# Performance work log

Measured on AMD Instinct MI355X. Metric: run time of the kernel, lower is better.

## Reference

```python
import jax, jax.numpy as jnp
import numpy as np
from jax import lax

D_MODEL = 256
SCALES = 3
DM2 = 2 * D_MODEL            # 512, inner d_model of each Mamba2
EXPAND = 2
D_INNER = EXPAND * DM2       # 1024
HEADDIM = 64                 # Mamba2 default
NHEADS = D_INNER // HEADDIM  # 16
DSTATE = 128
DCONV = 4
D_IN_PROJ = 2 * D_INNER + 2 * DSTATE + NHEADS  # 2320
CONV_CH = D_INNER + 2 * DSTATE                 # 1280


def layernorm(x, g, b, eps=1e-5):
    mu = x.mean(-1, keepdims=True)
    v = ((x - mu) ** 2).mean(-1, keepdims=True)
    return (x - mu) * lax.rsqrt(v + eps) * g + b


def mamba2(x, Win, convw, convb, dtb, Alog, Dh, normw, Wout):
    # x: [B, L, DM2]
    Bb, L, _ = x.shape
    zxbcdt = x @ Win                                   # [B, L, 2320]
    z = zxbcdt[..., :D_INNER]                          # gate branch
    xBC = zxbcdt[..., D_INNER:D_INNER + CONV_CH]       # [B, L, 1280]
    dt = jax.nn.softplus(zxbcdt[..., -NHEADS:] + dtb)  # [B, L, H]
    # causal depthwise conv1d over time
    xc = lax.conv_general_dilated(
        xBC.transpose(0, 2, 1), convw[:, None, :], (1,), [(DCONV - 1, 0)],
        feature_group_count=CONV_CH, dimension_numbers=('NCH', 'OIH', 'NCH'))
    xBC = jax.nn.silu(xc.transpose(0, 2, 1) + convb)
    xs = xBC[..., :D_INNER].reshape(Bb, L, NHEADS, HEADDIM)  # [B,L,H,P]
    Bm = xBC[..., D_INNER:D_INNER + DSTATE]                  # [B,L,N] (ngroups=1)
    Cm = xBC[..., D_INNER + DSTATE:]                         # [B,L,N]
    A = -jnp.exp(Alog)                                       # [H]
    dA = jnp.exp(dt * A)                                     # [B,L,H]

    def step(h, inp):
        dA_t, dt_t, x_t, B_t, C_t = inp
        h = dA_t[:, :, None, None] * h + jnp.einsum('bh,bhp,bn->bhpn', dt_t, x_t, B_t)
        return h, jnp.einsum('bhpn,bn->bhp', h, C_t)

    h0 = jnp.zeros((Bb, NHEADS, HEADDIM, DSTATE), x.dtype)
    _, ys = lax.scan(step, h0, (dA.transpose(1, 0, 2), dt.transpose(1, 0, 2),
                                xs.transpose(1, 0, 2, 3), Bm.transpose(1, 0, 2),
                                Cm.transpose(1, 0, 2)))
    y = ys.transpose(1, 0, 2, 3) + Dh[None, None, :, None] * xs   # skip term
    y = y.reshape(Bb, L, D_INNER)
    y = y * jax.nn.silu(z)                                        # gated RMSNorm
    y = y * lax.rsqrt((y * y).mean(-1, keepdims=True) + 1e-5) * normw
    return y @ Wout


def msfusion(x, Wp, bp, Wpre, bpre, lnpre_g, lnpre_b, Wpost, bpost, lnpost_g, lnpost_b,
             Win_f, convw_f, convb_f, dtb_f, Alog_f, Dh_f, normw_f, Wout_f,
             Win_b, convw_b, convb_b, dtb_b, Alog_b, Dh_b, normw_b, Wout_b):
    B, S, T, D = x.shape
    x_ = x.transpose(0, 2, 1, 3).reshape(B, T, S * D)
    x_ = x_ @ Wp + bp                                  # 1x1 conv == linear
    shortcut = x_
    h = layernorm(x_ @ Wpre + bpre, lnpre_g, lnpre_b)  # [B,T,512]
    gate = jax.nn.silu(h)
    out_f = mamba2(h, Win_f, convw_f, convb_f, dtb_f, Alog_f, Dh_f, normw_f, Wout_f)
    out_b = jnp.flip(mamba2(jnp.flip(h, 1), Win_b, convw_b, convb_b, dtb_b, Alog_b, Dh_b, normw_b, Wout_b), 1)
    out = layernorm((out_f * gate + out_b * gate) @ Wpost + bpost, lnpost_g, lnpost_b) + shortcut
    fn = out / jnp.maximum(jnp.linalg.norm(out, axis=-1, keepdims=True), 1e-12)
    attn = jnp.einsum('btd,bsd->bts', fn, fn)          # [B,T,T]
    return out, attn


def setup_inputs() -> dict:
    key = jax.random.key(0)
    ks = iter(jax.random.split(key, 40))
    n = lambda shape, s=0.02: (s * jax.random.normal(next(ks), shape)).astype(jnp.float32)
    B, S, T, D = 4, SCALES, 2048, D_MODEL
    inp = {
        'x': jax.random.normal(next(ks), (B, S, T, D), jnp.float32),
        'Wp': n((S * D, D)), 'bp': n((D,)),
        'Wpre': n((D, DM2)), 'bpre': n((DM2,)),
        'lnpre_g': jnp.ones((DM2,), jnp.float32), 'lnpre_b': jnp.zeros((DM2,), jnp.float32),
        'Wpost': n((DM2, D)), 'bpost': n((D,)),
        'lnpost_g': jnp.ones((D,), jnp.float32), 'lnpost_b': jnp.zeros((D,), jnp.float32),
    }
    for sfx in ('f', 'b'):
        inp['Win_' + sfx] = n((DM2, D_IN_PROJ))
        inp['convw_' + sfx] = n((CONV_CH, DCONV), 0.1)
        inp['convb_' + sfx] = jnp.zeros((CONV_CH,), jnp.float32)
        inp['dtb_' + sfx] = n((NHEADS,), 0.5)
        inp['Alog_' + sfx] = jnp.log(jnp.arange(1, NHEADS + 1, dtype=jnp.float32))
        inp['Dh_' + sfx] = jnp.ones((NHEADS,), jnp.float32)
        inp['normw_' + sfx] = jnp.ones((D_INNER,), jnp.float32)
        inp['Wout_' + sfx] = n((D_INNER, DM2))
    return inp


def reference(x, Wp, bp, Wpre, bpre, lnpre_g, lnpre_b, Wpost, bpost, lnpost_g, lnpost_b,
              Win_f, convw_f, convb_f, dtb_f, Alog_f, Dh_f, normw_f, Wout_f,
              Win_b, convw_b, convb_b, dtb_b, Alog_b, Dh_b, normw_b, Wout_b):
    return msfusion(x, Wp, bp, Wpre, bpre, lnpre_g, lnpre_b, Wpost, bpost, lnpost_g, lnpost_b,
                    Win_f, convw_f, convb_f, dtb_f, Alog_f, Dh_f, normw_f, Wout_f,
                    Win_b, convw_b, convb_b, dtb_b, Alog_b, Dh_b, normw_b, Wout_b)
```

## Files before the change

### kernel.cpp

```cpp
#include <hip/hip_runtime.h>
#include <math.h>

__device__ __forceinline__ float sigf(float v) { return 1.f / (1.f + __expf(-v)); }

__device__ __forceinline__ short f2bf(float f) {
  unsigned int u = __builtin_bit_cast(unsigned int, f);
  unsigned int r = (u + 0x7fffu + ((u >> 16) & 1u)) >> 16;
  return (short)r;
}
__device__ __forceinline__ float bf2f(short s) {
  unsigned int u = ((unsigned int)(unsigned short)s) << 16;
  return __builtin_bit_cast(float, u);
}

typedef short bf16x8 __attribute__((ext_vector_type(8)));
typedef float f32x4 __attribute__((ext_vector_type(4)));

#define ZB_STRIDE   19005440ll
#define XCV_STRIDE  10485760ll
#define SBUF_STRIDE 16777216ll
#define YB_STRIDE    8388608ll
#define DT_STRIDE     131072ll
#define PB_STRIDE       2048ll

__device__ __forceinline__ void async16(const short* g, short* l) {
  __builtin_amdgcn_global_load_lds(
      (const __attribute__((address_space(1))) unsigned int*)g,
      (__attribute__((address_space(3))) unsigned int*)l, 16, 0, 0);
}

template<bool BIAS, bool ACC>
__global__ __launch_bounds__(256) void gemm16_kernel(
    const short* __restrict__ A, const short* __restrict__ Bt,
    const float* __restrict__ bias, float* __restrict__ C,
    int M, int N, int K, int ldc,
    long long sAb, long long sBb, long long sCb)
{
  __shared__ short sm[2][2][128 * 32];
  const int tid = threadIdx.x;
  const int wave = tid >> 6;
  const int lane = tid & 63;
  const int m0 = blockIdx.x * 128;
  const int n0 = blockIdx.y * 128;
  const int bz = blockIdx.z;
  const short* Ab = A + (size_t)bz * sAb;
  const short* Bb = Bt + (size_t)bz * sBb;
  float* Cb = C + (size_t)bz * sCb;

  f32x4 acc[4][4] = {};

  const int isB = wave >> 1;
  const int half = wave & 1;
  const short* gsrc = isB ? Bb : Ab;
  const int tile_r0 = isB ? n0 : m0;
  const int lrow = lane >> 2;
  const int lk = (((lane & 3) ^ ((lane >> 3) & 3)) * 8);
  const short* gbase = gsrc + (size_t)(tile_r0 + half * 64 + lrow) * K + lk;
  short* lbase0 = &sm[0][isB][(half * 64) * 32];
  short* lbase1 = &sm[1][isB][(half * 64) * 32];

  const int wm = wave >> 1, wn = wave & 1;
  const int nt = K >> 5;

  auto STAGE = [&](int buf, int t) {
    const short* g0 = gbase + t * 32;
    short* l0 = buf ? lbase1 : lbase0;
#pragma unroll
    for (int c = 0; c < 4; c++)
      async16(g0 + (size_t)c * 16 * K, l0 + c * 512);
  };

  STAGE(0, 0);
  asm volatile("s_waitcnt vmcnt(0)" ::: "memory");
  __builtin_amdgcn_s_barrier();

  const int rs = (((lane >> 4) ^ ((lane >> 1) & 3)) * 8);
  int cur = 0;
  for (int t = 0; t < nt; ++t) {
    if (t + 1 < nt) STAGE(cur ^ 1, t + 1);
    const short* smA = &sm[cur][0][0];
    const short* smB = &sm[cur][1][0];
    bf16x8 af[4], bfr[4];
#pragma unroll
    for (int mt = 0; mt < 4; mt++)
      af[mt] = *(bf16x8*)&smA[(wm * 64 + mt * 16 + (lane & 15)) * 32 + rs];
#pragma unroll
    for (int nn = 0; nn < 4; nn++)
      bfr[nn] = *(bf16x8*)&smB[(wn * 64 + nn * 16 + (lane & 15)) * 32 + rs];
#pragma unroll
    for (int mt = 0; mt < 4; mt++)
#pragma unroll
      for (int nn = 0; nn < 4; nn++)
        acc[mt][nn] = __builtin_amdgcn_mfma_f32_16x16x32_bf16(bfr[nn], af[mt], acc[mt][nn], 0, 0, 0);
    asm volatile("s_waitcnt vmcnt(0)" ::: "memory");
    __builtin_amdgcn_s_barrier();
    cur ^= 1;
  }
  const int mcol = lane & 15;
  const int nq = (lane >> 4) * 4;
#pragma unroll
  for (int mt = 0; mt < 4; mt++) {
    int row = m0 + wm * 64 + mt * 16 + mcol;
#pragma unroll
    for (int nn = 0; nn < 4; nn++) {
      int col = n0 + wn * 64 + nn * 16 + nq;
      if (col >= N) continue;
      float4 v = make_float4(acc[mt][nn][0], acc[mt][nn][1], acc[mt][nn][2], acc[mt][nn][3]);
      float* cp = Cb + (size_t)row * ldc + col;
      if (BIAS) {
        float4 bv = *(const float4*)(bias + col);
        v.x += bv.x; v.y += bv.y; v.z += bv.z; v.w += bv.w;
      }
      if (ACC) {
        float4 ov = *(const float4*)cp;
        v.x += ov.x; v.y += ov.y; v.z += ov.z; v.w += ov.w;
      }
      *(float4*)cp = v;
    }
  }
}

__global__ void tcast_kernel(const float* __restrict__ W, short* __restrict__ Wt,
                             int K, int N)
{
  __shared__ float tile[32][33];
  int n0 = blockIdx.x * 32, k0 = blockIdx.y * 32;
  int c = threadIdx.x & 31, r8 = threadIdx.x >> 5;
#pragma unroll
  for (int i = 0; i < 4; i++) {
    int r = r8 + i * 8;
    int n = n0 + c;
    tile[r][c] = (n < N) ? W[(size_t)(k0 + r) * N + n] : 0.f;
  }
  __syncthreads();
#pragma unroll
  for (int i = 0; i < 4; i++) {
    int r = r8 + i * 8;
    Wt[(size_t)(n0 + r) * K + k0 + c] = f2bf(tile[c][r]);
  }
}

__global__ void tcast2_kernel(const float* __restrict__ W0, const float* __restrict__ W1,
                              short* __restrict__ Wt, int K, int N, long long sWt)
{
  __shared__ float tile[32][33];
  const int dir = blockIdx.z;
  const float* W = dir ? W1 : W0;
  short* Wtd = Wt + (size_t)dir * sWt;
  int n0 = blockIdx.x * 32, k0 = blockIdx.y * 32;
  int c = threadIdx.x & 31, r8 = threadIdx.x >> 5;
#pragma unroll
  for (int i = 0; i < 4; i++) {
    int r = r8 + i * 8;
    int n = n0 + c;
    tile[r][c] = (n < N) ? W[(size_t)(k0 + r) * N + n] : 0.f;
  }
  __syncthreads();
#pragma unroll
  for (int i = 0; i < 4; i++) {
    int r = r8 + i * 8;
    Wtd[(size_t)(n0 + r) * K + k0 + c] = f2bf(tile[c][r]);
  }
}

__global__ void gather_cast_kernel(const float* __restrict__ x, short* __restrict__ Ag)
{
  int idx = blockIdx.x * 256 + threadIdx.x;
  int m = idx / 192;
  int g = idx - m * 192;
  int k = g * 4;
  int s = k >> 8, d = k & 255;
  int b = m >> 11, t = m & 2047;
  float4 v = *(const float4*)(x + ((size_t)((b * 3 + s) * 2048 + t) << 8) + d);
  *(short4*)(Ag + (size_t)m * 768 + k) = make_short4(f2bf(v.x), f2bf(v.y), f2bf(v.z), f2bf(v.w));
}

__global__ void cast_kernel(const float* __restrict__ in, short* __restrict__ out)
{
  size_t idx = (size_t)blockIdx.x * 256 + threadIdx.x;
  float4 v = *(const float4*)(in + idx * 4);
  *(short4*)(out + idx * 4) = make_short4(f2bf(v.x), f2bf(v.y), f2bf(v.z), f2bf(v.w));
}

__global__ void ln512_kernel(float* __restrict__ xio, const float* __restrict__ g,
                             const float* __restrict__ b, short* __restrict__ o16)
{
  const int row = blockIdx.x;
  const int lane = threadIdx.x;
  float* xr = xio + (size_t)row * 512;
  float4 v0 = *(float4*)(xr + lane * 4);
  float4 v1 = *(float4*)(xr + 256 + lane * 4);
  float sum = v0.x + v0.y + v0.z + v0.w + v1.x + v1.y + v1.z + v1.w;
#pragma unroll
  for (int o = 32; o >= 1; o >>= 1) sum += __shfl_xor(sum, o);
  const float mu = sum * (1.f / 512.f);
  float d[8] = {v0.x - mu, v0.y - mu, v0.z - mu, v0.w - mu,
                v1.x - mu, v1.y - mu, v1.z - mu, v1.w - mu};
  float vs = 0.f;
#pragma unroll
  for (int i = 0; i < 8; i++) vs += d[i] * d[i];
#pragma unroll
  for (int o = 32; o >= 1; o >>= 1) vs += __shfl_xor(vs, o);
  const float inv = rsqrtf(vs * (1.f / 512.f) + 1e-5f);
  float4 g0 = *(const float4*)(g + lane * 4);
  float4 g1 = *(const float4*)(g + 256 + lane * 4);
  float4 b0 = *(const float4*)(b + lane * 4);
  float4 b1 = *(const float4*)(b + 256 + lane * 4);
  v0.x = d[0] * inv * g0.x + b0.x; v0.y = d[1] * inv * g0.y + b0.y;
  v0.z = d[2] * inv * g0.z + b0.z; v0.w = d[3] * inv * g0.w + b0.w;
  v1.x = d[4] * inv * g1.x + b1.x; v1.y = d[5] * inv * g1.y + b1.y;
  v1.z = d[6] * inv * g1.z + b1.z; v1.w = d[7] * inv * g1.w + b1.w;
  *(float4*)(xr + lane * 4) = v0;
  *(float4*)(xr + 256 + lane * 4) = v1;
  short* orow = o16 + (size_t)row * 512;
  *(short4*)(orow + lane * 4) = make_short4(f2bf(v0.x), f2bf(v0.y), f2bf(v0.z), f2bf(v0.w));
  *(short4*)(orow + 256 + lane * 4) = make_short4(f2bf(v1.x), f2bf(v1.y), f2bf(v1.z), f2bf(v1.w));
}

__global__ void dtprep_kernel(const float* __restrict__ Z,
                              const float* __restrict__ dtb0, const float* __restrict__ dtb1,
                              const float* __restrict__ Alog0, const float* __restrict__ Alog1,
                              float* __restrict__ dtv, float* __restrict__ ldA)
{
  const int dir = blockIdx.y;
  const float* Zd = Z + (size_t)dir * ZB_STRIDE;
  const float* dtb = dir ? dtb1 : dtb0;
  const float* Alog = dir ? Alog1 : Alog0;
  float* dtvd = dtv + dir * DT_STRIDE;
  float* ldAd = ldA + dir * DT_STRIDE;
  int idx = blockIdx.x * 256 + threadIdx.x;
  int row = idx >> 4, hh = idx & 15;
  float raw = Zd[(size_t)row * 2320 + 2304 + hh] + dtb[hh];
  float dt = raw > 20.f ? raw : log1pf(expf(raw));
  dtvd[idx] = dt;
  ldAd[idx] = -dt * expf(Alog[hh]);
}

__global__ void conv_kernel(const float* __restrict__ Z,
                            const float* __restrict__ cw0, const float* __restrict__ cw1,
                            const float* __restrict__ cb0, const float* __restrict__ cb1,
                            short* __restrict__ xcv)
{
  const int dir = blockIdx.z;
  const int t0 = blockIdx.x * 64;
  const int b = blockIdx.y / 5;
  const int chb = blockIdx.y % 5;
  const int c = chb * 256 + threadIdx.x;
  const float* convw = dir ? cw1 : cw0;
  const float* convb = dir ? cb1 : cb0;
  const float* Zd = Z + (size_t)dir * ZB_STRIDE + (size_t)(b * 2048) * 2320 + 1024 + c;
  short* xd = xcv + (size_t)dir * XCV_STRIDE + (size_t)(b * 2048) * 1280 + c;

  const float w0 = convw[c * 4 + 0], w1 = convw[c * 4 + 1];
  const float w2 = convw[c * 4 + 2], w3 = convw[c * 4 + 3];
  const float bias = convb[c];
  const int o = dir ? 0 : -3;

  float rr[4];
#pragma unroll
  for (int j = 0; j < 4; j++) {
    int pos = t0 + o + j;
    rr[j] = (pos >= 0 && pos < 2048) ? Zd[(size_t)pos * 2320] : 0.f;
  }
#pragma unroll 8
  for (int i = 0; i < 64; i++) {
    float a = bias;
    if (dir) { a += w0 * rr[3]; a += w1 * rr[2]; a += w2 * rr[1]; a += w3 * rr[0]; }
    else     { a += w0 * rr[0]; a += w1 * rr[1]; a += w2 * rr[2]; a += w3 * rr[3]; }
    xd[(size_t)(t0 + i) * 1280] = f2bf(a * sigf(a));
    rr[0] = rr[1]; rr[1] = rr[2]; rr[2] = rr[3];
    int pos = t0 + i + 1 + o + 3;
    rr[3] = (pos >= 0 && pos < 2048) ? Zd[(size_t)pos * 2320] : 0.f;
  }
}

__global__ __launch_bounds__(256) void chunk_state_kernel(
    const short* __restrict__ xcv_, const float* __restrict__ dtv_,
    const float* __restrict__ ldA_, short* __restrict__ Sbuf_,
    float* __restrict__ Pbuf_)
{
  __shared__ float sw[64];
  __shared__ short sXT[64 * 74];
  __shared__ short sBw[128 * 74];
  const int dir = blockIdx.z;
  const short* xcv = xcv_ + (size_t)dir * XCV_STRIDE;
  const float* dtv = dtv_ + dir * DT_STRIDE;
  const float* ldA = ldA_ + dir * DT_STRIDE;
  short* Sbuf = Sbuf_ + (size_t)dir * SBUF_STRIDE;
  float* Pbuf = Pbuf_ + dir * PB_STRIDE;
  const int bh = blockIdx.x, ck = blockIdx.y;
  const int b = bh >> 4, h = bh & 15;
  const int tid = threadIdx.x;
  const int wave = tid >> 6, lane = tid & 63;

  if (tid < 64) {
    int tg = ck * 64 + tid;
    int tt = dir ? 2047 - tg : tg;
    size_t r = (size_t)(b * 2048 + tt) * 16 + h;
    float v = ldA[r];
#pragma unroll
    for (int o = 1; o < 64; o <<= 1) { float u = __shfl_up(v, o); if (tid >= o) v += u; }
    float tot = __shfl(v, 63);
    sw[tid] = __expf(tot - v) * dtv[r];
    if (tid == 63) Pbuf[bh * 32 + ck] = __expf(tot);
  }
  __syncthreads();
  for (int i4 = tid; i4 < 512; i4 += 256) {
    int s = i4 >> 3, p0 = (i4 & 7) * 8;
    int tg = ck * 64 + s; int tt = dir ? 2047 - tg : tg;
    bf16x8 xv = *(const bf16x8*)(xcv + (size_t)(b * 2048 + tt) * 1280 + h * 64 + p0);
#pragma unroll
    for (int j = 0; j < 8; j++) sXT[(p0 + j) * 74 + s] = xv[j];
  }
  for (int i4 = tid; i4 < 1024; i4 += 256) {
    int s = i4 >> 4, n0 = (i4 & 15) * 8;
    int tg = ck * 64 + s; int tt = dir ? 2047 - tg : tg;
    bf16x8 bv = *(const bf16x8*)(xcv + (size_t)(b * 2048 + tt) * 1280 + 1024 + n0);
    float w = sw[s];
#pragma unroll
    for (int j = 0; j < 8; j++) sBw[(n0 + j) * 74 + s] = f2bf(w * bf2f(bv[j]));
  }
  __syncthreads();

  const int mcol = lane & 15, kgrp = (lane >> 4) * 8;
  bf16x8 af[2];
#pragma unroll
  for (int kk = 0; kk < 2; kk++)
    af[kk] = *(bf16x8*)&sXT[(wave * 16 + mcol) * 74 + kk * 32 + kgrp];
  f32x4 acc[8] = {};
#pragma unroll
  for (int j = 0; j < 8; j++)
#pragma unroll
    for (int kk = 0; kk < 2; kk++) {
      bf16x8 bf = *(bf16x8*)&sBw[(j * 16 + mcol) * 74 + kk * 32 + kgrp];
      acc[j] = __builtin_amdgcn_mfma_f32_16x16x32_bf16(bf, af[kk], acc[j], 0, 0, 0);
    }
  short* Sp = Sbuf + ((size_t)(bh * 32 + ck) << 13);
  const int p = wave * 16 + mcol;
  const int nq = (lane >> 4) * 4;
#pragma unroll
  for (int j = 0; j < 8; j++) {
    *(short4*)(Sp + p * 128 + j * 16 + nq) = make_short4(
        f2bf(acc[j][0]), f2bf(acc[j][1]), f2bf(acc[j][2]), f2bf(acc[j][3]));
  }
}

__global__ void chunk_scan_kernel(short* __restrict__ Sbuf, const float* __restrict__ Pbuf)
{
  int idx = blockIdx.x * 256 + threadIdx.x;
  int bhd = idx >> 12;
  int pr = idx & 4095;
  int dir = bhd >> 6, bh = bhd & 63;
  short* Sb = Sbuf + (size_t)dir * SBUF_STRIDE;
  const float* Pb = Pbuf + dir * PB_STRIDE;
  float h0 = 0.f, h1 = 0.f;
  for (int ck = 0; ck < 32; ck++) {
    size_t off = ((size_t)(bh * 32 + ck) << 13) + pr * 2;
    unsigned int u = *(const unsigned int*)(Sb + off);
    float s0 = bf2f((short)(u & 0xffff));
    float s1 = bf2f((short)(u >> 16));
    float P = Pb[bh * 32 + ck];
    unsigned int w = (unsigned int)(unsigned short)f2bf(h0) |
                     ((unsigned int)(unsigned short)f2bf(h1) << 16);
    *(unsigned int*)(Sb + off) = w;
    h0 = P * h0 + s0;
    h1 = P * h1 + s1;
  }
}

__global__ __launch_bounds__(256) void chunk_out_kernel(
    const short* __restrict__ xcv_, const float* __restrict__ dtv_,
    const float* __restrict__ ldA_, const short* __restrict__ Sbuf_,
    const float* __restrict__ Dh0, const float* __restrict__ Dh1,
    short* __restrict__ y_)
{
  extern __shared__ short smem16[];
  short* sB  = smem16;
  short* sXT = sB + 64 * 136;
  short* sP  = sXT + 64 * 74;
  float* sL  = (float*)(sP + 64 * 74);
  float* sdt = sL + 64;

  const int dir = blockIdx.z;
  const short* xcv = xcv_ + (size_t)dir * XCV_STRIDE;
  const float* dtv = dtv_ + dir * DT_STRIDE;
  const float* ldA = ldA_ + dir * DT_STRIDE;
  const short* Sbuf = Sbuf_ + (size_t)dir * SBUF_STRIDE;
  const float* Dh = dir ? Dh1 : Dh0;
  short* y = y_ + (size_t)dir * YB_STRIDE;

  const int bh = blockIdx.x, ck = blockIdx.y;
  const int b = bh >> 4, h = bh & 15;
  const int tid = threadIdx.x;
  const int wave = tid >> 6, lane = tid & 63;

  const int mcol = lane & 15;
  const int kgrp = (lane >> 4) * 8;
  const int trow = wave * 16 + mcol;
  const int sq = (lane >> 4) * 4;

  const int tgc = ck * 64 + trow;
  const int ttc = dir ? 2047 - tgc : tgc;
  const short* crow = xcv + (size_t)(b * 2048 + ttc) * 1280 + 1152;
  bf16x8 afC[4];
#pragma unroll
  for (int kk = 0; kk < 4; kk++)
    afC[kk] = *(const bf16x8*)(crow + kk * 32 + kgrp);

  if (tid < 64) {
    int tg = ck * 64 + tid;
    int tt = dir ? 2047 - tg : tg;
    size_t r = (size_t)(b * 2048 + tt) * 16 + h;
    float v = ldA[r];
#pragma unroll
    for (int o = 1; o < 64; o <<= 1) { float u = __shfl_up(v, o); if (tid >= o) v += u; }
    sL[tid] = v;
    sdt[tid] = dtv[r];
  }
  for (int i4 = tid; i4 < 1024; i4 += 256) {
    int t = i4 >> 4, c8 = (i4 & 15) * 8;
    int tg = ck * 64 + t; int tt = dir ? 2047 - tg : tg;
    const short* rp = xcv + (size_t)(b * 2048 + tt) * 1280;
    *(bf16x8*)&sB[t * 136 + c8] = *(const bf16x8*)(rp + 1024 + c8);
  }
  for (int i4 = tid; i4 < 512; i4 += 256) {
    int t = i4 >> 3, p0 = (i4 & 7) * 8;
    int tg = ck * 64 + t; int tt = dir ? 2047 - tg : tg;
    bf16x8 xv = *(const bf16x8*)(xcv + (size_t)(b * 2048 + tt) * 1280 + h * 64 + p0);
#pragma unroll
    for (int j = 0; j < 8; j++) sXT[(p0 + j) * 74 + t] = xv[j];
  }
  __syncthreads();

  f32x4 sacc[4] = {};
#pragma unroll
  for (int j = 0; j < 4; j++)
#pragma unroll
    for (int kk = 0; kk < 4; kk++) {
      bf16x8 bf = *(bf16x8*)&sB[(j * 16 + mcol) * 136 + kk * 32 + kgrp];
      sacc[j] = __builtin_amdgcn_mfma_f32_16x16x32_bf16(bf, afC[kk], sacc[j], 0, 0, 0);
    }

  const float Lt = sL[trow];
#pragma unroll
  for (int j = 0; j < 4; j++) {
    int s0 = j * 16 + sq;
    float vr[4];
#pragma unroll
    for (int r = 0; r < 4; r++) {
      int s = s0 + r;
      vr[r] = (trow >= s) ? sacc[j][r] * __expf(Lt - sL[s]) * sdt[s] : 0.f;
    }
    *(short4*)&sP[trow * 74 + s0] = make_short4(
        f2bf(vr[0]), f2bf(vr[1]), f2bf(vr[2]), f2bf(vr[3]));
  }
  asm volatile("s_waitcnt lgkmcnt(0)" ::: "memory");
  __builtin_amdgcn_sched_barrier(0);

  bf16x8 afP[2];
#pragma unroll
  for (int kk = 0; kk < 2; kk++)
    afP[kk] = *(bf16x8*)&sP[trow * 74 + kk * 32 + kgrp];
  f32x4 yacc[4] = {};
#pragma unroll
  for (int j = 0; j < 4; j++)
#pragma unroll
    for (int kk = 0; kk < 2; kk++) {
      bf16x8 bf = *(bf16x8*)&sXT[(j * 16 + mcol) * 74 + kk * 32 + kgrp];
      yacc[j] = __builtin_amdgcn_mfma_f32_16x16x32_bf16(bf, afP[kk], yacc[j], 0, 0, 0);
    }
  const short* Hp = Sbuf + ((size_t)(bh * 32 + ck) << 13);
  f32x4 y2[4] = {};
#pragma unroll
  for (int j = 0; j < 4; j++)
#pragma unroll
    for (int kk = 0; kk < 4; kk++) {
      bf16x8 bf = *(const bf16x8*)(Hp + (j * 16 + mcol) * 128 + kk * 32 + kgrp);
      y2[j] = __builtin_amdgcn_mfma_f32_16x16x32_bf16(bf, afC[kk], y2[j], 0, 0, 0);
    }

  const float dh = Dh[h];
  const float eL = __expf(Lt);
  short* yrow = y + (size_t)(b * 2048 + ttc) * 1024 + h * 64;
#pragma unroll
  for (int j = 0; j < 4; j++) {
    int p0 = j * 16 + sq;
    short o[4];
#pragma unroll
    for (int r = 0; r < 4; r++) {
      float xv = bf2f(sXT[(p0 + r) * 74 + trow]);
      o[r] = f2bf(yacc[j][r] + eL * y2[j][r] + dh * xv);
    }
    *(short4*)(yrow + p0) = make_short4(o[0], o[1], o[2], o[3]);
  }
}

__global__ void rms_kernel(short* __restrict__ y_, const float* __restrict__ Z,
                           const float* __restrict__ nw0, const float* __restrict__ nw1)
{
  const int dir = blockIdx.y;
  const int row = blockIdx.x;
  const int lane = threadIdx.x;
  short* yr = y_ + (size_t)dir * YB_STRIDE + (size_t)row * 1024;
  const float* zr = Z + (size_t)dir * ZB_STRIDE + (size_t)row * 2320;
  const float* normw = dir ? nw1 : nw0;
  float vals[16];
  float ss = 0.f;
#pragma unroll
  for (int jj = 0; jj < 4; jj++) {
    int off = jj * 256 + lane * 4;
    short4 yv = *(short4*)(yr + off);
    float4 zv = *(const float4*)(zr + off);
    float a0 = bf2f(yv.x) * (zv.x * sigf(zv.x));
    float a1 = bf2f(yv.y) * (zv.y * sigf(zv.y));
    float a2 = bf2f(yv.z) * (zv.z * sigf(zv.z));
    float a3 = bf2f(yv.w) * (zv.w * sigf(zv.w));
    vals[jj * 4 + 0] = a0; vals[jj * 4 + 1] = a1;
    vals[jj * 4 + 2] = a2; vals[jj * 4 + 3] = a3;
    ss += a0 * a0 + a1 * a1 + a2 * a2 + a3 * a3;
  }
#pragma unroll
  for (int o = 32; o >= 1; o >>= 1) ss += __shfl_xor(ss, o);
  const float scale = rsqrtf(ss * (1.f / 1024.f) + 1e-5f);
#pragma unroll
  for (int jj = 0; jj < 4; jj++) {
    int off = jj * 256 + lane * 4;
    float4 nw = *(const float4*)(normw + off);
    *(short4*)(yr + off) = make_short4(
        f2bf(vals[jj * 4 + 0] * scale * nw.x), f2bf(vals[jj * 4 + 1] * scale * nw.y),
        f2bf(vals[jj * 4 + 2] * scale * nw.z), f2bf(vals[jj * 4 + 3] * scale * nw.w));
  }
}

__global__ void combine_kernel(const float* __restrict__ od, const float* __restrict__ h,
                               short* __restrict__ ob)
{
  size_t idx = (size_t)blockIdx.x * 256 + threadIdx.x;
  float4 o = ((const float4*)od)[idx];
  float4 g = ((const float4*)h)[idx];
  o.x *= g.x * sigf(g.x);
  o.y *= g.y * sigf(g.y);
  o.z *= g.z * sigf(g.z);
  o.w *= g.w * sigf(g.w);
  *(short4*)(ob + idx * 4) = make_short4(f2bf(o.x), f2bf(o.y), f2bf(o.z), f2bf(o.w));
}

__global__ void lnshort_kernel(const float* __restrict__ v, const float* __restrict__ g,
                               const float* __restrict__ b, const float* __restrict__ shortcut,
                               float* __restrict__ out0, short* __restrict__ fn)
{
  const int row = blockIdx.x;
  const int lane = threadIdx.x;
  size_t base = (size_t)row * 256;
  float4 x = *(const float4*)(v + base + lane * 4);
  float sum = x.x + x.y + x.z + x.w;
#pragma unroll
  for (int o = 32; o >= 1; o >>= 1) sum += __shfl_xor(sum, o);
  const float mu = sum * (1.f / 256.f);
  float d[4] = {x.x - mu, x.y - mu, x.z - mu, x.w - mu};
  float vs = d[0] * d[0] + d[1] * d[1] + d[2] * d[2] + d[3] * d[3];
#pragma unroll
  for (int o = 32; o >= 1; o >>= 1) vs += __shfl_xor(vs, o);
  const float inv = rsqrtf(vs * (1.f / 256.f) + 1e-5f);
  float4 gg = *(const float4*)(g + lane * 4);
  float4 bb = *(const float4*)(b + lane * 4);
  float4 sc = *(const float4*)(shortcut + base + lane * 4);
  float4 o4;
  o4.x = d[0] * inv * gg.x + bb.x + sc.x;
  o4.y = d[1] * inv * gg.y + bb.y + sc.y;
  o4.z = d[2] * inv * gg.z + bb.z + sc.z;
  o4.w = d[3] * inv * gg.w + bb.w + sc.w;
  *(float4*)(out0 + base + lane * 4) = o4;
  float ns = o4.x * o4.x + o4.y * o4.y + o4.z * o4.z + o4.w * o4.w;
#pragma unroll
  for (int o = 32; o >= 1; o >>= 1) ns += __shfl_xor(ns, o);
  const float r = 1.f / fmaxf(sqrtf(ns), 1e-12f);
  *(short4*)(fn + base + lane * 4) =
      make_short4(f2bf(o4.x * r), f2bf(o4.y * r), f2bf(o4.z * r), f2bf(o4.w * r));
}

extern "C" void kernel_launch(void* const* d_in, const int* in_sizes, int n_in,
                              void* d_out, int out_size, void* d_ws, size_t ws_size,
                              hipStream_t stream)
{
  (void)in_sizes; (void)n_in; (void)out_size; (void)ws_size;
  const float* x        = (const float*)d_in[0];
  const float* Wp       = (const float*)d_in[1];
  const float* bp       = (const float*)d_in[2];
  const float* Wpre     = (const float*)d_in[3];
  const float* bpre     = (const float*)d_in[4];
  const float* lnpre_g  = (const float*)d_in[5];
  const float* lnpre_b  = (const float*)d_in[6];
  const float* Wpost    = (const float*)d_in[7];
  const float* bpost    = (const float*)d_in[8];
  const float* lnpost_g = (const float*)d_in[9];
  const float* lnpost_b = (const float*)d_in[10];
  const float* Win_f   = (const float*)d_in[11];
  const float* convw_f = (const float*)d_in[12];
  const float* convb_f = (const float*)d_in[13];
  const float* dtb_f   = (const float*)d_in[14];
  const float* Alog_f  = (const float*)d_in[15];
  const float* Dh_f    = (const float*)d_in[16];
  const float* normw_f = (const float*)d_in[17];
  const float* Wout_f  = (const float*)d_in[18];
  const float* Win_b   = (const float*)d_in[19];
  const float* convw_b = (const float*)d_in[20];
  const float* convb_b = (const float*)d_in[21];
  const float* dtb_b   = (const float*)d_in[22];
  const float* Alog_b  = (const float*)d_in[23];
  const float* Dh_b    = (const float*)d_in[24];
  const float* normw_b = (const float*)d_in[25];
  const float* Wout_b  = (const float*)d_in[26];

  float* ws   = (float*)d_ws;
  float* Zb   = ws;
  float* xcvr = Zb + 2 * 19005440;
  float* xc   = xcvr + 10485760;
  float* hbuf = xc + 2097152;
  short* hb16 = (short*)(hbuf + 4194304);
  float* yb16f= hbuf + 4194304 + 2097152;
  short* yb16 = (short*)yb16f;
  float* od   = yb16f + 8388608;
  float* dtv  = od + 4194304;
  float* ldA  = dtv + 262144;
  float* Pbuf = ldA + 262144;
  short* WinT = (short*)(Pbuf + 4096);
  short* WoutT= WinT + 2 * 1245184;

  short* xcv16  = (short*)xcvr;
  short* Ag16   = (short*)xcvr;
  short* WpT    = (short*)(xcvr + 3145728);
  short* xcb    = (short*)xcvr;
  short* WpreT  = (short*)(xcvr + 1048576);
  short* ob16   = (short*)xcvr;
  short* WpostT = (short*)(xcvr + 2097152);
  float* vbuf = yb16f;
  short* fn16 = (short*)(yb16f + 2097152);

  float* out0 = (float*)d_out;
  float* attn = out0 + 2097152;
  short* Sbuf16 = (short*)attn;

  tcast_kernel<<<dim3(8, 24), 256, 0, stream>>>(Wp, WpT, 768, 256);
  gather_cast_kernel<<<6144, 256, 0, stream>>>(x, Ag16);
  gemm16_kernel<true, false><<<dim3(64, 2), 256, 0, stream>>>(Ag16, WpT, bp, xc, 8192, 256, 768, 256, 0, 0, 0);
  cast_kernel<<<2048, 256, 0, stream>>>(xc, xcb);
  tcast_kernel<<<dim3(16, 8), 256, 0, stream>>>(Wpre, WpreT, 256, 512);
  gemm16_kernel<true, false><<<dim3(64, 4), 256, 0, stream>>>(xcb, WpreT, bpre, hbuf, 8192, 512, 256, 512, 0, 0, 0);
  ln512_kernel<<<8192, 64, 0, stream>>>(hbuf, lnpre_g, lnpre_b, hb16);

  tcast2_kernel<<<dim3(76, 16, 2), 256, 0, stream>>>(Win_f, Win_b, WinT, 512, 2320, 1245184);
  tcast2_kernel<<<dim3(16, 32, 2), 256, 0, stream>>>(Wout_f, Wout_b, WoutT, 1024, 512, 524288);
  gemm16_kernel<false, false><<<dim3(64, 19, 2), 256, 0, stream>>>(
      hb16, WinT, nullptr, Zb, 8192, 2320, 512, 2320, 0, 1245184, ZB_STRIDE);
  dtprep_kernel<<<dim3(512, 2), 256, 0, stream>>>(Zb, dtb_f, dtb_b, Alog_f, Alog_b, dtv, ldA);
  conv_kernel<<<dim3(32, 20, 2), 256, 0, stream>>>(Zb, convw_f, convw_b, convb_f, convb_b, xcv16);
  chunk_state_kernel<<<dim3(64, 32, 2), 256, 0, stream>>>(xcv16, dtv, ldA, Sbuf16, Pbuf);
  chunk_scan_kernel<<<2048, 256, 0, stream>>>(Sbuf16, Pbuf);
  chunk_out_kernel<<<dim3(64, 32, 2), 256, 36864, stream>>>(xcv16, dtv, ldA, Sbuf16, Dh_f, Dh_b, yb16);
  rms_kernel<<<dim3(8192, 2), 64, 0, stream>>>(yb16, Zb, normw_f, normw_b);
  gemm16_kernel<false, false><<<dim3(64, 4), 256, 0, stream>>>(yb16, WoutT, nullptr, od, 8192, 512, 1024, 512, 0, 0, 0);
  gemm16_kernel<false, true><<<dim3(64, 4), 256, 0, stream>>>(yb16 + YB_STRIDE, WoutT + 524288, nullptr, od, 8192, 512, 1024, 512, 0, 0, 0);

  combine_kernel<<<4096, 256, 0, stream>>>(od, hbuf, ob16);
  tcast_kernel<<<dim3(8, 16), 256, 0, stream>>>(Wpost, WpostT, 512, 256);
  gemm16_kernel<true, false><<<dim3(64, 2), 256, 0, stream>>>(ob16, WpostT, bpost, vbuf, 8192, 256, 512, 256, 0, 0, 0);
  lnshort_kernel<<<8192, 64, 0, stream>>>(vbuf, lnpost_g, lnpost_b, xc, out0, fn16);
  gemm16_kernel<false, false><<<dim3(16, 16, 4), 256, 0, stream>>>(
      fn16, fn16, nullptr, attn, 2048, 2048, 256, 2048,
      (long long)2048 * 256, (long long)2048 * 256, (long long)2048 * 2048);
}
```

Measured before the change: 550.9 us.

## Add 256x256 triple-buffered GEMM for in-proj and attention, fuse casts

Adds a 512-thread GEMM kernel with 256x256 tiles and a three-stage async LDS pipeline, and uses it for the large Mamba in-projection (padding the transposed weight stride to 2560 columns) and the batched self-attention product. The first projection GEMM now writes a bf16 copy directly, which removes a separate cast kernel. The two out-projection GEMMs write separate buffers that the combine kernel sums, dropping the read-modify-write accumulate pass. Larger tiles raise operand reuse but cut the number of blocks and add register and LDS pressure.

New measurement: 555.8 us. About the same (+0.9%).

```diff
diff --git a/kernel.cpp b/kernel.cpp
--- a/kernel.cpp
+++ b/kernel.cpp
@@ -22,6 +22,7 @@
 #define YB_STRIDE    8388608ll
 #define DT_STRIDE     131072ll
 #define PB_STRIDE       2048ll
+#define WINT_STRIDE  1310720ll
 
 __device__ __forceinline__ void async16(const short* g, short* l) {
   __builtin_amdgcn_global_load_lds(
@@ -29,12 +30,112 @@
       (__attribute__((address_space(3))) unsigned int*)l, 16, 0, 0);
 }
 
-template<bool BIAS, bool ACC>
+template<bool BIAS>
+__global__ __launch_bounds__(512, 2) void gemm256_kernel(
+    const short* __restrict__ A, const short* __restrict__ Bt,
+    const float* __restrict__ bias, float* __restrict__ C,
+    int M, int N, int K, int ldc,
+    long long sAb, long long sBb, long long sCb)
+{
+  __shared__ short smA[3][256 * 32];
+  __shared__ short smB[3][256 * 32];
+  const int tid = threadIdx.x;
+  const int w = tid >> 6;
+  const int lane = tid & 63;
+  const int m0 = blockIdx.x * 256;
+  const int n0 = blockIdx.y * 256;
+  const short* Ab = A + (size_t)blockIdx.z * sAb;
+  const short* Bb = Bt + (size_t)blockIdx.z * sBb;
+  float* Cb = C + (size_t)blockIdx.z * sCb;
+
+  const int wm = w >> 2, wn = w & 3;
+  const int NT = K >> 5;
+
+  const int gs8 = (((tid & 3) ^ ((tid >> 3) & 3)) * 8);
+  const int r0 = tid >> 2;
+  const int lb = (w * 16) * 32;
+  const short* gA = Ab + (size_t)(m0 + r0) * K + gs8;
+  const short* gB = Bb + (size_t)(n0 + r0) * K + gs8;
+
+  auto STAGE_A = [&](int buf, int t) {
+    async16(gA + t * 32, &smA[buf][lb]);
+    async16(gA + (size_t)128 * K + t * 32, &smA[buf][lb + 128 * 32]);
+  };
+  auto STAGE_B = [&](int buf, int t) {
+    async16(gB + t * 32, &smB[buf][lb]);
+    async16(gB + (size_t)128 * K + t * 32, &smB[buf][lb + 128 * 32]);
+  };
+
+  f32x4 acc[8][4] = {};
+  const int mcol = lane & 15;
+  const int nq = (lane >> 4) * 4;
+  const int rs8 = (((lane >> 4) ^ ((lane >> 1) & 3)) * 8);
+
+  STAGE_A(0, 0); STAGE_B(0, 0);
+  if (NT > 1) { STAGE_A(1, 1); STAGE_B(1, 1); }
+  if (NT > 1) asm volatile("s_waitcnt vmcnt(4)" ::: "memory");
+  else        asm volatile("s_waitcnt vmcnt(0)" ::: "memory");
+  __builtin_amdgcn_s_barrier();
+
+  int cur = 0;
+  for (int t = 0; t < NT; ++t) {
+    int buf2 = cur + 2; if (buf2 >= 3) buf2 -= 3;
+    const short* sa = smA[cur];
+    const short* sb = smB[cur];
+    bf16x8 bfr[4], af[4];
+#pragma unroll
+    for (int nt = 0; nt < 4; nt++)
+      bfr[nt] = *(bf16x8*)&sb[(wn * 64 + nt * 16 + mcol) * 32 + rs8];
+#pragma unroll
+    for (int mt = 0; mt < 4; mt++)
+      af[mt] = *(bf16x8*)&sa[(wm * 128 + mt * 16 + mcol) * 32 + rs8];
+    if (t + 2 < NT) STAGE_A(buf2, t + 2);
+#pragma unroll
+    for (int mt = 0; mt < 4; mt++)
+#pragma unroll
+      for (int nt = 0; nt < 4; nt++)
+        acc[mt][nt] = __builtin_amdgcn_mfma_f32_16x16x32_bf16(bfr[nt], af[mt], acc[mt][nt], 0, 0, 0);
+#pragma unroll
+    for (int mt = 0; mt < 4; mt++)
+      af[mt] = *(bf16x8*)&sa[(wm * 128 + 64 + mt * 16 + mcol) * 32 + rs8];
+    if (t + 2 < NT) STAGE_B(buf2, t + 2);
+#pragma unroll
+    for (int mt = 0; mt < 4; mt++)
+#pragma unroll
+      for (int nt = 0; nt < 4; nt++)
+        acc[4 + mt][nt] = __builtin_amdgcn_mfma_f32_16x16x32_bf16(bfr[nt], af[mt], acc[4 + mt][nt], 0, 0, 0);
+    if (t + 1 < NT) {
+      if (t + 2 < NT) asm volatile("s_waitcnt vmcnt(4)" ::: "memory");
+      else            asm volatile("s_waitcnt vmcnt(0)" ::: "memory");
+      __builtin_amdgcn_s_barrier();
+    }
+    cur = (cur + 1 == 3) ? 0 : cur + 1;
+  }
+
+#pragma unroll
+  for (int mt = 0; mt < 8; mt++) {
+    int row = m0 + wm * 128 + (mt >> 2) * 64 + (mt & 3) * 16 + mcol;
+#pragma unroll
+    for (int nt = 0; nt < 4; nt++) {
+      int col = n0 + wn * 64 + nt * 16 + nq;
+      if (col >= N) continue;
+      float4 v = make_float4(acc[mt][nt][0], acc[mt][nt][1], acc[mt][nt][2], acc[mt][nt][3]);
+      if (BIAS) {
+        float4 bv = *(const float4*)(bias + col);
+        v.x += bv.x; v.y += bv.y; v.z += bv.z; v.w += bv.w;
+      }
+      *(float4*)(Cb + (size_t)row * ldc + col) = v;
+    }
+  }
+}
+
+template<bool BIAS, bool ACC, bool W16>
 __global__ __launch_bounds__(256) void gemm16_kernel(
     const short* __restrict__ A, const short* __restrict__ Bt,
     const float* __restrict__ bias, float* __restrict__ C,
     int M, int N, int K, int ldc,
-    long long sAb, long long sBb, long long sCb)
+    long long sAb, long long sBb, long long sCb,
+    short* __restrict__ C16)
 {
   __shared__ short sm[2][2][128 * 32];
   const int tid = threadIdx.x;
@@ -116,6 +217,10 @@
         v.x += ov.x; v.y += ov.y; v.z += ov.z; v.w += ov.w;
       }
       *(float4*)cp = v;
+      if (W16) {
+        *(short4*)(C16 + (size_t)row * ldc + col) =
+            make_short4(f2bf(v.x), f2bf(v.y), f2bf(v.z), f2bf(v.w));
+      }
     }
   }
 }
@@ -173,13 +278,6 @@
   int b = m >> 11, t = m & 2047;
   float4 v = *(const float4*)(x + ((size_t)((b * 3 + s) * 2048 + t) << 8) + d);
   *(short4*)(Ag + (size_t)m * 768 + k) = make_short4(f2bf(v.x), f2bf(v.y), f2bf(v.z), f2bf(v.w));
-}
-
-__global__ void cast_kernel(const float* __restrict__ in, short* __restrict__ out)
-{
-  size_t idx = (size_t)blockIdx.x * 256 + threadIdx.x;
-  float4 v = *(const float4*)(in + idx * 4);
-  *(short4*)(out + idx * 4) = make_short4(f2bf(v.x), f2bf(v.y), f2bf(v.z), f2bf(v.w));
 }
 
 __global__ void ln512_kernel(float* __restrict__ xio, const float* __restrict__ g,
@@ -532,16 +630,18 @@
   }
 }
 
-__global__ void combine_kernel(const float* __restrict__ od, const float* __restrict__ h,
-                               short* __restrict__ ob)
+__global__ void combine_kernel(const float* __restrict__ od0, const float* __restrict__ od1,
+                               const float* __restrict__ h, short* __restrict__ ob)
 {
   size_t idx = (size_t)blockIdx.x * 256 + threadIdx.x;
-  float4 o = ((const float4*)od)[idx];
+  float4 a = ((const float4*)od0)[idx];
+  float4 bb = ((const float4*)od1)[idx];
   float4 g = ((const float4*)h)[idx];
-  o.x *= g.x * sigf(g.x);
-  o.y *= g.y * sigf(g.y);
-  o.z *= g.z * sigf(g.z);
-  o.w *= g.w * sigf(g.w);
+  float4 o;
+  o.x = (a.x + bb.x) * (g.x * sigf(g.x));
+  o.y = (a.y + bb.y) * (g.y * sigf(g.y));
+  o.z = (a.z + bb.z) * (g.z * sigf(g.z));
+  o.w = (a.w + bb.w) * (g.w * sigf(g.w));
   *(short4*)(ob + idx * 4) = make_short4(f2bf(o.x), f2bf(o.y), f2bf(o.z), f2bf(o.w));
 }
 
@@ -625,7 +725,7 @@
   float* ldA  = dtv + 262144;
   float* Pbuf = ldA + 262144;
   short* WinT = (short*)(Pbuf + 4096);
-  short* WoutT= WinT + 2 * 1245184;
+  short* WoutT= WinT + 2 * WINT_STRIDE;
 
   short* xcv16  = (short*)xcvr;
   short* Ag16   = (short*)xcvr;
@@ -640,33 +740,38 @@
   float* out0 = (float*)d_out;
   float* attn = out0 + 2097152;
   short* Sbuf16 = (short*)attn;
+  float* od1 = attn;
 
   tcast_kernel<<<dim3(8, 24), 256, 0, stream>>>(Wp, WpT, 768, 256);
   gather_cast_kernel<<<6144, 256, 0, stream>>>(x, Ag16);
-  gemm16_kernel<true, false><<<dim3(64, 2), 256, 0, stream>>>(Ag16, WpT, bp, xc, 8192, 256, 768, 256, 0, 0, 0);
-  cast_kernel<<<2048, 256, 0, stream>>>(xc, xcb);
+  gemm16_kernel<true, false, true><<<dim3(64, 2), 256, 0, stream>>>(
+      Ag16, WpT, bp, xc, 8192, 256, 768, 256, 0, 0, 0, xcb);
   tcast_kernel<<<dim3(16, 8), 256, 0, stream>>>(Wpre, WpreT, 256, 512);
-  gemm16_kernel<true, false><<<dim3(64, 4), 256, 0, stream>>>(xcb, WpreT, bpre, hbuf, 8192, 512, 256, 512, 0, 0, 0);
+  gemm16_kernel<true, false, false><<<dim3(64, 4), 256, 0, stream>>>(
+      xcb, WpreT, bpre, hbuf, 8192, 512, 256, 512, 0, 0, 0, nullptr);
   ln512_kernel<<<8192, 64, 0, stream>>>(hbuf, lnpre_g, lnpre_b, hb16);
 
-  tcast2_kernel<<<dim3(76, 16, 2), 256, 0, stream>>>(Win_f, Win_b, WinT, 512, 2320, 1245184);
+  tcast2_kernel<<<dim3(80, 16, 2), 256, 0, stream>>>(Win_f, Win_b, WinT, 512, 2320, WINT_STRIDE);
   tcast2_kernel<<<dim3(16, 32, 2), 256, 0, stream>>>(Wout_f, Wout_b, WoutT, 1024, 512, 524288);
-  gemm16_kernel<false, false><<<dim3(64, 19, 2), 256, 0, stream>>>(
-      hb16, WinT, nullptr, Zb, 8192, 2320, 512, 2320, 0, 1245184, ZB_STRIDE);
+  gemm256_kernel<false><<<dim3(32, 10, 2), 512, 0, stream>>>(
+      hb16, WinT, nullptr, Zb, 8192, 2320, 512, 2320, 0, WINT_STRIDE, ZB_STRIDE);
   dtprep_kernel<<<dim3(512, 2), 256, 0, stream>>>(Zb, dtb_f, dtb_b, Alog_f, Alog_b, dtv, ldA);
   conv_kernel<<<dim3(32, 20, 2), 256, 0, stream>>>(Zb, convw_f, convw_b, convb_f, convb_b, xcv16);
   chunk_state_kernel<<<dim3(64, 32, 2), 256, 0, stream>>>(xcv16, dtv, ldA, Sbuf16, Pbuf);
   chunk_scan_kernel<<<2048, 256, 0, stream>>>(Sbuf16, Pbuf);
   chunk_out_kernel<<<dim3(64, 32, 2), 256, 36864, stream>>>(xcv16, dtv, ldA, Sbuf16, Dh_f, Dh_b, yb16);
   rms_kernel<<<dim3(8192, 2), 64, 0, stream>>>(yb16, Zb, normw_f, normw_b);
-  gemm16_kernel<false, false><<<dim3(64, 4), 256, 0, stream>>>(yb16, WoutT, nullptr, od, 8192, 512, 1024, 512, 0, 0, 0);
-  gemm16_kernel<false, true><<<dim3(64, 4), 256, 0, stream>>>(yb16 + YB_STRIDE, WoutT + 524288, nullptr, od, 8192, 512, 1024, 512, 0, 0, 0);
-
-  combine_kernel<<<4096, 256, 0, stream>>>(od, hbuf, ob16);
+  gemm16_kernel<false, false, false><<<dim3(64, 4), 256, 0, stream>>>(
+      yb16, WoutT, nullptr, od, 8192, 512, 1024, 512, 0, 0, 0, nullptr);
+  gemm16_kernel<false, false, false><<<dim3(64, 4), 256, 0, stream>>>(
+      yb16 + YB_STRIDE, WoutT + 524288, nullptr, od1, 8192, 512, 1024, 512, 0, 0, 0, nullptr);
+
+  combine_kernel<<<4096, 256, 0, stream>>>(od, od1, hbuf, ob16);
   tcast_kernel<<<dim3(8, 16), 256, 0, stream>>>(Wpost, WpostT, 512, 256);
-  gemm16_kernel<true, false><<<dim3(64, 2), 256, 0, stream>>>(ob16, WpostT, bpost, vbuf, 8192, 256, 512, 256, 0, 0, 0);
+  gemm16_kernel<true, false, false><<<dim3(64, 2), 256, 0, stream>>>(
+      ob16, WpostT, bpost, vbuf, 8192, 256, 512, 256, 0, 0, 0, nullptr);
   lnshort_kernel<<<8192, 64, 0, stream>>>(vbuf, lnpost_g, lnpost_b, xc, out0, fn16);
-  gemm16_kernel<false, false><<<dim3(16, 16, 4), 256, 0, stream>>>(
+  gemm256_kernel<false><<<dim3(8, 8, 4), 512, 0, stream>>>(
       fn16, fn16, nullptr, attn, 2048, 2048, 256, 2048,
       (long long)2048 * 256, (long long)2048 * 256, (long long)2048 * 2048);
 }
```
